# Kernel optimization log

Measured on AMD Instinct MI355X. Metric: run time of the kernel, lower is better.

Reference implementation:

```python
import jax, jax.numpy as jnp
import numpy as np

B, T, D = 64, 512, 2048
N = 16384            # buffer_size
ROUNDS = 10          # max_replay_rounds
DECAY = 0.9
THR = 0.5            # priority_threshold


def setup_inputs() -> dict:
    key = jax.random.key(0)
    ks = jax.random.split(key, 6)
    s = 0.02
    return {
        "query_states": jax.random.normal(ks[0], (B, T, D), jnp.float32),
        "attention_mask": jnp.ones((B, T), jnp.float32),
        "keys": jax.random.normal(ks[1], (N, D), jnp.float32),
        "values": jax.random.normal(ks[2], (N, D), jnp.float32),
        "priorities": jax.random.uniform(ks[3], (N,), jnp.float32),
        "ages": jnp.zeros((N,), jnp.float32),
        "valid_mask": jnp.ones((N,), jnp.bool_),
        "Wq": jax.random.normal(ks[4], (D, D), jnp.float32) * s,
        "bq": jnp.zeros((D,), jnp.float32),
        "Wc": jax.random.normal(ks[5], (D, D), jnp.float32) * s,
        "bc": jnp.zeros((D,), jnp.float32),
    }


def reference(query_states, attention_mask, keys, values, priorities, ages,
              valid_mask, Wq, bq, Wc, bc):
    # Masked mean-pool of context -> query  (B, D)
    m = attention_mask[..., None]
    query = (query_states * m).sum(axis=1) / (m.sum(axis=1) + 1e-8)
    query = query @ Wq.T + bq

    validf = valid_mask.astype(query.dtype)
    inv_sqrt_d = 1.0 / jnp.sqrt(jnp.asarray(D, query.dtype))
    base_scores = (query @ keys.T) * inv_sqrt_d  # (B, N), reused every round
    round_w = DECAY ** jnp.arange(ROUNDS, dtype=query.dtype)

    def step(carry, rw):
        w_ages, stopped, acc, wsum = carry
        eff = priorities * (DECAY ** w_ages)                       # (N,)
        active = jax.nn.sigmoid((eff - THR) * 10.0) * validf       # (N,)
        stopped = jnp.logical_or(stopped, active.sum() < 0.5)
        inc = jnp.where(stopped, 0.0, 1.0).astype(query.dtype)
        scores = base_scores * (active * eff)[None, :]             # (B, N)
        scores = jnp.where(valid_mask[None, :], scores, -jnp.inf)
        aw = jax.nn.softmax(scores, axis=-1)                       # (B, N)
        out = aw @ values                                          # (B, D)
        acc = acc + inc * rw * out
        wsum = wsum + inc * rw
        w_ages = w_ages + inc * jax.lax.stop_gradient(aw.mean(axis=0))
        return (w_ages, stopped, acc, wsum), None

    init = (ages, jnp.asarray(False), jnp.zeros((B, D), query.dtype),
            jnp.asarray(0.0, query.dtype))
    (w_ages, stopped, acc, wsum), _ = jax.lax.scan(step, init, round_w)

    # round_weights are normalized over the rounds actually executed
    consolidated = acc / jnp.maximum(wsum, 1e-8)
    consolidated = consolidated @ Wc.T + bc
    # if no round ran (or buffer empty), output is zeros (no projection)
    return jnp.where(wsum > 0, consolidated, jnp.zeros_like(consolidated))
```

## Files before the change

### kernel.cpp

```cpp
#include <hip/hip_runtime.h>
#include <math.h>

#define BB 64
#define TT 512
#define DD 2048
#define NBUF 16384
#define RND 10
#define DEC 0.9f
#define LN_DEC -0.10536051565782628f
#define THRV 0.5f
#define RBLK 64

constexpr size_t OFF_L    = 0;
constexpr size_t OFF_ASUM = OFF_L + (size_t)RND * BB;
constexpr size_t OFF_BAR  = OFF_ASUM + RND;
constexpr size_t ZERO_FLOATS = OFF_BAR + 4;
constexpr size_t OFF_ATOT = 656;
constexpr size_t OFF_BASE = OFF_ATOT + (size_t)BB * NBUF;
constexpr size_t OFF_ACC  = OFF_BASE + (size_t)BB * NBUF;
constexpr size_t OFF_POOL = OFF_ACC + (size_t)BB * DD;
constexpr size_t OFF_Q    = OFF_POOL + (size_t)BB * DD;
constexpr size_t OFF_MSUM = OFF_Q + (size_t)BB * DD;
constexpr size_t OFF_VLD  = OFF_MSUM + 64;
constexpr size_t OFF_PART = OFF_VLD + NBUF;
constexpr size_t WS_FLOATS = OFF_PART + (size_t)8 * BB * DD;

__device__ __forceinline__ float wave_sum(float v) {
#pragma unroll
  for (int o = 32; o; o >>= 1) v += __shfl_down(v, o);
  return v;
}

__device__ __forceinline__ float dev_wsum(const float* asum) {
  bool stopped = false; float w = 1.f, s = 0.f;
#pragma unroll
  for (int r = 0; r < RND; r++) {
    if (asum[r] < 0.5f) stopped = true;
    if (!stopped) s += w;
    w *= DEC;
  }
  return s;
}

__global__ __launch_bounds__(256) void k_valid(const void* __restrict__ valid, float* __restrict__ ws) {
  const unsigned char* vb = (const unsigned char*)valid;
  const unsigned int* vw = (const unsigned int*)valid;
  bool byte_layout = true;
#pragma unroll
  for (int i = 0; i < 16; i++) byte_layout = byte_layout && (vb[i] == (unsigned char)1);
  int n = blockIdx.x * 256 + threadIdx.x;
  float v = byte_layout ? (vb[n] ? 1.f : 0.f) : (vw[n] ? 1.f : 0.f);
  ws[OFF_VLD + n] = v;
}

__global__ __launch_bounds__(256) void k_msum(const float* __restrict__ mask, float* __restrict__ ws) {
  float* msum = ws + OFF_MSUM;
  int b = blockIdx.x, t = threadIdx.x;
  float s = mask[b * TT + t] + mask[b * TT + t + 256];
  s = wave_sum(s);
  __shared__ float red[4];
  if ((t & 63) == 0) red[t >> 6] = s;
  __syncthreads();
  if (t == 0) msum[b] = red[0] + red[1] + red[2] + red[3];
}

__global__ __launch_bounds__(256) void k_pool(const float* __restrict__ qs, const float* __restrict__ mask,
                                              float* __restrict__ ws) {
  float* part = ws + OFF_PART;
  int b = blockIdx.y;
  int d0 = blockIdx.x * 1024 + threadIdx.x * 4;
  int t0 = blockIdx.z * 64;
  __shared__ float ms[64];
  if (threadIdx.x < 64) ms[threadIdx.x] = mask[b * TT + t0 + threadIdx.x];
  __syncthreads();
  const float* p = qs + ((size_t)b * TT + t0) * DD + d0;
  float4 acc = make_float4(0.f, 0.f, 0.f, 0.f);
#pragma unroll 4
  for (int t = 0; t < 64; t++) {
    float m = ms[t];
    float4 v = *(const float4*)(p + (size_t)t * DD);
    acc.x = fmaf(v.x, m, acc.x); acc.y = fmaf(v.y, m, acc.y);
    acc.z = fmaf(v.z, m, acc.z); acc.w = fmaf(v.w, m, acc.w);
  }
  *(float4*)(part + ((size_t)blockIdx.z * BB + b) * DD + d0) = acc;
}

__global__ __launch_bounds__(256) void k_pooldiv(float* __restrict__ ws) {
  size_t i = (size_t)blockIdx.x * 256 + threadIdx.x;
  const float* part = ws + OFF_PART;
  const float* msum = ws + OFF_MSUM;
  float* pooled = ws + OFF_POOL;
  size_t BD = (size_t)BB * DD;
  float s = 0.f;
#pragma unroll
  for (int c = 0; c < 8; c++) s += part[c * BD + i];
  int b = (int)(i >> 11);
  pooled[i] = s / (msum[b] + 1e-8f);
}

__device__ __forceinline__ void stage_t(float* __restrict__ dst, const float* __restrict__ src, int ld) {
  int tr = threadIdx.x >> 2;
  int kb = (threadIdx.x & 3) << 4;
  const float* s = src + (size_t)tr * ld + kb;
#pragma unroll
  for (int q = 0; q < 4; q++) {
    float4 v = *(const float4*)(s + q * 4);
    int k = kb + q * 4;
    dst[(k + 0) * 68 + tr] = v.x;
    dst[(k + 1) * 68 + tr] = v.y;
    dst[(k + 2) * 68 + tr] = v.z;
    dst[(k + 3) * 68 + tr] = v.w;
  }
}

__device__ __forceinline__ void stage_t_bias(float* __restrict__ dst, const float* __restrict__ src, int ld,
                                             const float* __restrict__ bias) {
  int tr = threadIdx.x >> 2;
  int kb = (threadIdx.x & 3) << 4;
  const float* s = src + (size_t)tr * ld + kb;
#pragma unroll
  for (int q = 0; q < 4; q++) {
    float4 v = *(const float4*)(s + q * 4);
    float4 bv = *(const float4*)(bias + kb + q * 4);
    v.x += bv.x; v.y += bv.y; v.z += bv.z; v.w += bv.w;
    int k = kb + q * 4;
    dst[(k + 0) * 68 + tr] = v.x;
    dst[(k + 1) * 68 + tr] = v.y;
    dst[(k + 2) * 68 + tr] = v.z;
    dst[(k + 3) * 68 + tr] = v.w;
  }
}

__device__ __forceinline__ void stage_t_scale(float* __restrict__ dst, const float* __restrict__ src, int ld,
                                              float sc) {
  int tr = threadIdx.x >> 2;
  int kb = (threadIdx.x & 3) << 4;
  const float* s = src + (size_t)tr * ld + kb;
#pragma unroll
  for (int q = 0; q < 4; q++) {
    float4 v = *(const float4*)(s + q * 4);
    int k = kb + q * 4;
    dst[(k + 0) * 68 + tr] = v.x * sc;
    dst[(k + 1) * 68 + tr] = v.y * sc;
    dst[(k + 2) * 68 + tr] = v.z * sc;
    dst[(k + 3) * 68 + tr] = v.w * sc;
  }
}

__device__ __forceinline__ void stage_n(float* __restrict__ dst, const float* __restrict__ src, int ld) {
  int tr = threadIdx.x >> 2;
  int db = (threadIdx.x & 3) << 4;
  const float* s = src + (size_t)tr * ld + db;
  float* d = dst + tr * 68 + db;
#pragma unroll
  for (int q = 0; q < 4; q++) *(float4*)(d + q * 4) = *(const float4*)(s + q * 4);
}

__device__ __forceinline__ void gemm_core(const float* __restrict__ At, const float* __restrict__ Bt,
                                          float (&c)[4][4]) {
  const int tx = (threadIdx.x & 15) * 4;
  const int ty = (threadIdx.x >> 4) * 4;
#pragma unroll
  for (int k = 0; k < 64; k++) {
    float4 a = *(const float4*)(At + k * 68 + ty);
    float4 b = *(const float4*)(Bt + k * 68 + tx);
    c[0][0] = fmaf(a.x, b.x, c[0][0]); c[0][1] = fmaf(a.x, b.y, c[0][1]);
    c[0][2] = fmaf(a.x, b.z, c[0][2]); c[0][3] = fmaf(a.x, b.w, c[0][3]);
    c[1][0] = fmaf(a.y, b.x, c[1][0]); c[1][1] = fmaf(a.y, b.y, c[1][1]);
    c[1][2] = fmaf(a.y, b.z, c[1][2]); c[1][3] = fmaf(a.y, b.w, c[1][3]);
    c[2][0] = fmaf(a.z, b.x, c[2][0]); c[2][1] = fmaf(a.z, b.y, c[2][1]);
    c[2][2] = fmaf(a.z, b.z, c[2][2]); c[2][3] = fmaf(a.z, b.w, c[2][3]);
    c[3][0] = fmaf(a.w, b.x, c[3][0]); c[3][1] = fmaf(a.w, b.y, c[3][1]);
    c[3][2] = fmaf(a.w, b.z, c[3][2]); c[3][3] = fmaf(a.w, b.w, c[3][3]);
  }
}

__global__ __launch_bounds__(256) void k_wq(const float* __restrict__ Wq, float* __restrict__ ws) {
  __shared__ float At[64 * 68], Bt[64 * 68];
  const float* pooled = ws + OFF_POOL;
  float* part = ws + OFF_PART;
  int j0 = blockIdx.x * 64;
  int kc = blockIdx.y * 256;
  float c[4][4] = {};
  for (int kb = 0; kb < 256; kb += 64) {
    __syncthreads();
    stage_t(At, pooled + kc + kb, DD);
    stage_t(Bt, Wq + (size_t)j0 * DD + kc + kb, DD);
    __syncthreads();
    gemm_core(At, Bt, c);
  }
  int tx = (threadIdx.x & 15) * 4, ty = (threadIdx.x >> 4) * 4;
#pragma unroll
  for (int ii = 0; ii < 4; ii++) {
    float4 v = make_float4(c[ii][0], c[ii][1], c[ii][2], c[ii][3]);
    *(float4*)(part + ((size_t)blockIdx.y * BB + ty + ii) * DD + j0 + tx) = v;
  }
}

__global__ __launch_bounds__(256) void k_red8(float* __restrict__ dst, const float* __restrict__ ws) {
  size_t i = (size_t)blockIdx.x * 256 + threadIdx.x;
  const float* part = ws + OFF_PART;
  size_t BD = (size_t)BB * DD;
  float s = 0.f;
#pragma unroll
  for (int c = 0; c < 8; c++) s += part[c * BD + i];
  dst[i] = s;
}

__global__ __launch_bounds__(256) void k_base(const float* __restrict__ keys, const float* __restrict__ bq,
                                              float* __restrict__ ws) {
  __shared__ float At[64 * 68], Bt[64 * 68];
  const float* qacc = ws + OFF_Q;
  float* base = ws + OFF_BASE;
  int n0 = blockIdx.x * 64;
  float c[4][4] = {};
  for (int kb = 0; kb < DD; kb += 64) {
    __syncthreads();
    stage_t_bias(At, qacc + kb, DD, bq + kb);
    stage_t(Bt, keys + (size_t)n0 * DD + kb, DD);
    __syncthreads();
    gemm_core(At, Bt, c);
  }
  const float sc = 0.022097086912079608f;
  int tx = (threadIdx.x & 15) * 4, ty = (threadIdx.x >> 4) * 4;
#pragma unroll
  for (int ii = 0; ii < 4; ii++) {
    float4 v = make_float4(c[ii][0] * sc, c[ii][1] * sc, c[ii][2] * sc, c[ii][3] * sc);
    *(float4*)(base + (size_t)(ty + ii) * NBUF + n0 + tx) = v;
  }
}

__global__ __launch_bounds__(1024) void k_rounds(const float* __restrict__ prior,
                                                 const float* __restrict__ ages,
                                                 float* __restrict__ ws) {
  __shared__ float base_sh[64 * 256];
  __shared__ float wsh[256];
  __shared__ float red[4][256];
  __shared__ float red2[64][4];
  __shared__ float asq[4];
  __shared__ float rlsh[64];
  __shared__ float ash;
  float* lrow = ws + OFF_L;
  float* asum = ws + OFF_ASUM;
  unsigned int* bar = (unsigned int*)(ws + OFF_BAR);
  float* Atot = ws + OFF_ATOT;
  const float* base = ws + OFF_BASE;
  const float* vldbuf = ws + OFF_VLD;

  const int tid = threadIdx.x;
  const int nl = tid & 255, bq = tid >> 8;
  const int lane = tid & 63, sub = (tid >> 6) & 3;
  const int bx = blockIdx.x;
  const int n = bx * 256 + nl;

#pragma unroll
  for (int i = 0; i < 4; i++) {
    int f = (i * 1024 + tid) * 4;
    int b = f >> 8, c = f & 255;
    *(float4*)(base_sh + b * 256 + c) = *(const float4*)(base + (size_t)b * NBUF + bx * 256 + c);
  }
  if (tid < 256) wsh[tid] = ages[bx * 256 + tid];
  const float pv = prior[n];
  const float vld = vldbuf[n];
  float atot[16];
#pragma unroll
  for (int i = 0; i < 16; i++) atot[i] = 0.f;
  float w = 1.f;
  bool stopped = false;
  __syncthreads();

  for (int r = 0; r < RND; r++) {
    const float wa = wsh[nl];
    const float eff = pv * __expf(wa * LN_DEC);
    const float act = vld / (1.f + __expf(-10.f * (eff - THRV)));
    const float g = act * eff;
#pragma unroll
    for (int bi = 0; bi < 16; bi++) {
      const int b = bq * 16 + bi;
      float e = vld * __expf(base_sh[b * 256 + nl] * g);
      e = wave_sum(e);
      if (lane == 0) red2[b][sub] = e;
    }
    if (bq == 0) {
      float s = wave_sum(act);
      if (lane == 0) asq[sub] = s;
    }
    __syncthreads();
    if (tid < 64) {
      __hip_atomic_fetch_add(lrow + (size_t)r * BB + tid,
                             red2[tid][0] + red2[tid][1] + red2[tid][2] + red2[tid][3],
                             __ATOMIC_RELEASE, __HIP_MEMORY_SCOPE_AGENT);
    } else if (tid == 64) {
      __hip_atomic_fetch_add(asum + r, asq[0] + asq[1] + asq[2] + asq[3],
                             __ATOMIC_RELEASE, __HIP_MEMORY_SCOPE_AGENT);
    }
    __syncthreads();
    if (tid == 0) {
      __hip_atomic_fetch_add(bar, 1u, __ATOMIC_RELEASE, __HIP_MEMORY_SCOPE_AGENT);
      const unsigned int target = (unsigned int)RBLK * (unsigned int)(r + 1);
      while (__hip_atomic_load(bar, __ATOMIC_ACQUIRE, __HIP_MEMORY_SCOPE_AGENT) < target)
        __builtin_amdgcn_s_sleep(2);
    }
    __syncthreads();
    if (tid < 64)
      rlsh[tid] = 1.f / __hip_atomic_load(lrow + (size_t)r * BB + tid,
                                          __ATOMIC_RELAXED, __HIP_MEMORY_SCOPE_AGENT);
    else if (tid == 64)
      ash = __hip_atomic_load(asum + r, __ATOMIC_RELAXED, __HIP_MEMORY_SCOPE_AGENT);
    __syncthreads();
    stopped = stopped || (ash < 0.5f);
    const float coef = stopped ? 0.f : w;
    const float inc = stopped ? 0.f : 1.f;
    float csum = 0.f;
#pragma unroll
    for (int bi = 0; bi < 16; bi++) {
      const int b = bq * 16 + bi;
      const float e = vld * __expf(base_sh[b * 256 + nl] * g);
      const float aw = e * rlsh[b];
      atot[bi] = fmaf(coef, aw, atot[bi]);
      csum += aw;
    }
    red[bq][nl] = csum;
    __syncthreads();
    if (bq == 0)
      wsh[nl] = wa + inc * (red[0][nl] + red[1][nl] + red[2][nl] + red[3][nl]) * (1.f / 64.f);
    w *= DEC;
    __syncthreads();
  }
#pragma unroll
  for (int bi = 0; bi < 16; bi++) {
    const int b = bq * 16 + bi;
    Atot[(size_t)b * NBUF + n] = atot[bi];
  }
}

__global__ __launch_bounds__(256) void k_pv(const float* __restrict__ values, float* __restrict__ ws) {
  __shared__ float At[64 * 68], Bt[64 * 68];
  const float* Atot = ws + OFF_ATOT;
  float* part = ws + OFF_PART;
  int d0 = blockIdx.x * 64;
  int nc = blockIdx.y * 2048;
  float c[4][4] = {};
  for (int kb = 0; kb < 2048; kb += 64) {
    __syncthreads();
    stage_t(At, Atot + nc + kb, NBUF);
    stage_n(Bt, values + (size_t)(nc + kb) * DD + d0, DD);
    __syncthreads();
    gemm_core(At, Bt, c);
  }
  int tx = (threadIdx.x & 15) * 4, ty = (threadIdx.x >> 4) * 4;
#pragma unroll
  for (int ii = 0; ii < 4; ii++) {
    float4 v = make_float4(c[ii][0], c[ii][1], c[ii][2], c[ii][3]);
    *(float4*)(part + ((size_t)blockIdx.y * BB + ty + ii) * DD + d0 + tx) = v;
  }
}

__global__ __launch_bounds__(256) void k_wc(const float* __restrict__ Wc, float* __restrict__ ws) {
  __shared__ float At[64 * 68], Bt[64 * 68];
  const float* acc = ws + OFF_ACC;
  float rws = 1.f / fmaxf(dev_wsum(ws + OFF_ASUM), 1e-8f);
  float* part = ws + OFF_PART;
  int j0 = blockIdx.x * 64;
  int kc = blockIdx.y * 256;
  float c[4][4] = {};
  for (int kb = 0; kb < 256; kb += 64) {
    __syncthreads();
    stage_t_scale(At, acc + kc + kb, DD, rws);
    stage_t(Bt, Wc + (size_t)j0 * DD + kc + kb, DD);
    __syncthreads();
    gemm_core(At, Bt, c);
  }
  int tx = (threadIdx.x & 15) * 4, ty = (threadIdx.x >> 4) * 4;
#pragma unroll
  for (int ii = 0; ii < 4; ii++) {
    float4 v = make_float4(c[ii][0], c[ii][1], c[ii][2], c[ii][3]);
    *(float4*)(part + ((size_t)blockIdx.y * BB + ty + ii) * DD + j0 + tx) = v;
  }
}

__global__ __launch_bounds__(256) void k_red8_fin(float* __restrict__ out, const float* __restrict__ bc,
                                                  const float* __restrict__ ws) {
  size_t i = (size_t)blockIdx.x * 256 + threadIdx.x;
  const float* part = ws + OFF_PART;
  size_t BD = (size_t)BB * DD;
  float s = 0.f;
#pragma unroll
  for (int c = 0; c < 8; c++) s += part[c * BD + i];
  float wsv = dev_wsum(ws + OFF_ASUM);
  int j = (int)(i & (DD - 1));
  out[i] = (wsv > 0.f) ? (s + bc[j]) : 0.f;
}

extern "C" void kernel_launch(void* const* d_in, const int* in_sizes, int n_in,
                              void* d_out, int out_size, void* d_ws, size_t ws_size,
                              hipStream_t stream) {
  (void)in_sizes; (void)n_in; (void)out_size; (void)ws_size;
  const float* qs    = (const float*)d_in[0];
  const float* mask  = (const float*)d_in[1];
  const float* keys  = (const float*)d_in[2];
  const float* vals  = (const float*)d_in[3];
  const float* prior = (const float*)d_in[4];
  const float* ages  = (const float*)d_in[5];
  const void*  valid = (const void*)d_in[6];
  const float* Wq = (const float*)d_in[7];
  const float* bq = (const float*)d_in[8];
  const float* Wc = (const float*)d_in[9];
  const float* bc = (const float*)d_in[10];
  float* out = (float*)d_out;
  float* ws  = (float*)d_ws;

  hipMemsetAsync(ws, 0, ZERO_FLOATS * sizeof(float), stream);

  k_valid<<<NBUF / 256, 256, 0, stream>>>(valid, ws);
  k_msum<<<BB, 256, 0, stream>>>(mask, ws);
  k_pool<<<dim3(2, BB, 8), 256, 0, stream>>>(qs, mask, ws);
  k_pooldiv<<<(BB * DD) / 256, 256, 0, stream>>>(ws);
  k_wq<<<dim3(32, 8), 256, 0, stream>>>(Wq, ws);
  k_red8<<<(BB * DD) / 256, 256, 0, stream>>>(ws + OFF_Q, ws);
  k_base<<<NBUF / 64, 256, 0, stream>>>(keys, bq, ws);
  k_rounds<<<RBLK, 1024, 0, stream>>>(prior, ages, ws);
  k_pv<<<dim3(32, 8), 256, 0, stream>>>(vals, ws);
  k_red8<<<(BB * DD) / 256, 256, 0, stream>>>(ws + OFF_ACC, ws);
  k_wc<<<dim3(32, 8), 256, 0, stream>>>(Wc, ws);
  k_red8_fin<<<(BB * DD) / 256, 256, 0, stream>>>(out, bc, ws);
}
```

Baseline: 885.8 us.

## Split-K the base and PV GEMMs, vectorize reductions, merge init kernels

The keys GEMM is split four ways along K (4x more blocks), with a new reduction kernel that sums the partials and applies the scale. The PV GEMM's K split goes from 8 to 32 chunks, reduced by a new 32-way kernel. All partial-sum reductions now use float4 loads and stores, and the mask-sum and valid-conversion kernels are merged into one launch. The aim is better GPU occupancy on the two largest GEMMs and fewer launches, at the cost of extra workspace traffic for the partial buffers.

```diff
diff --git a/kernel.cpp b/kernel.cpp
--- a/kernel.cpp
+++ b/kernel.cpp
@@ -23,7 +23,8 @@
 constexpr size_t OFF_MSUM = OFF_Q + (size_t)BB * DD;
 constexpr size_t OFF_VLD  = OFF_MSUM + 64;
 constexpr size_t OFF_PART = OFF_VLD + NBUF;
-constexpr size_t WS_FLOATS = OFF_PART + (size_t)8 * BB * DD;
+constexpr size_t OFF_BPART= OFF_PART + (size_t)32 * BB * DD;
+constexpr size_t WS_FLOATS = OFF_BPART + (size_t)4 * BB * NBUF;
 
 __device__ __forceinline__ float wave_sum(float v) {
 #pragma unroll
@@ -42,26 +43,27 @@
   return s;
 }
 
-__global__ __launch_bounds__(256) void k_valid(const void* __restrict__ valid, float* __restrict__ ws) {
-  const unsigned char* vb = (const unsigned char*)valid;
-  const unsigned int* vw = (const unsigned int*)valid;
-  bool byte_layout = true;
-#pragma unroll
-  for (int i = 0; i < 16; i++) byte_layout = byte_layout && (vb[i] == (unsigned char)1);
-  int n = blockIdx.x * 256 + threadIdx.x;
-  float v = byte_layout ? (vb[n] ? 1.f : 0.f) : (vw[n] ? 1.f : 0.f);
-  ws[OFF_VLD + n] = v;
-}
-
-__global__ __launch_bounds__(256) void k_msum(const float* __restrict__ mask, float* __restrict__ ws) {
-  float* msum = ws + OFF_MSUM;
-  int b = blockIdx.x, t = threadIdx.x;
-  float s = mask[b * TT + t] + mask[b * TT + t + 256];
-  s = wave_sum(s);
-  __shared__ float red[4];
-  if ((t & 63) == 0) red[t >> 6] = s;
-  __syncthreads();
-  if (t == 0) msum[b] = red[0] + red[1] + red[2] + red[3];
+__global__ __launch_bounds__(256) void k_init(const float* __restrict__ mask, const void* __restrict__ valid,
+                                              float* __restrict__ ws) {
+  if (blockIdx.x < 64) {
+    float* msum = ws + OFF_MSUM;
+    int b = blockIdx.x, t = threadIdx.x;
+    float s = mask[b * TT + t] + mask[b * TT + t + 256];
+    s = wave_sum(s);
+    __shared__ float red[4];
+    if ((t & 63) == 0) red[t >> 6] = s;
+    __syncthreads();
+    if (t == 0) msum[b] = red[0] + red[1] + red[2] + red[3];
+  } else {
+    const unsigned char* vb = (const unsigned char*)valid;
+    const unsigned int* vw = (const unsigned int*)valid;
+    bool byte_layout = true;
+#pragma unroll
+    for (int i = 0; i < 16; i++) byte_layout = byte_layout && (vb[i] == (unsigned char)1);
+    int n = (blockIdx.x - 64) * 256 + threadIdx.x;
+    float v = byte_layout ? (vb[n] ? 1.f : 0.f) : (vw[n] ? 1.f : 0.f);
+    ws[OFF_VLD + n] = v;
+  }
 }
 
 __global__ __launch_bounds__(256) void k_pool(const float* __restrict__ qs, const float* __restrict__ mask,
@@ -86,16 +88,21 @@
 }
 
 __global__ __launch_bounds__(256) void k_pooldiv(float* __restrict__ ws) {
-  size_t i = (size_t)blockIdx.x * 256 + threadIdx.x;
-  const float* part = ws + OFF_PART;
+  size_t i4 = (size_t)blockIdx.x * 256 + threadIdx.x;
+  const float4* part = (const float4*)(ws + OFF_PART);
   const float* msum = ws + OFF_MSUM;
-  float* pooled = ws + OFF_POOL;
-  size_t BD = (size_t)BB * DD;
-  float s = 0.f;
-#pragma unroll
-  for (int c = 0; c < 8; c++) s += part[c * BD + i];
-  int b = (int)(i >> 11);
-  pooled[i] = s / (msum[b] + 1e-8f);
+  float4* pooled = (float4*)(ws + OFF_POOL);
+  size_t BD4 = (size_t)BB * DD / 4;
+  float4 s = make_float4(0.f, 0.f, 0.f, 0.f);
+#pragma unroll
+  for (int c = 0; c < 8; c++) {
+    float4 v = part[c * BD4 + i4];
+    s.x += v.x; s.y += v.y; s.z += v.z; s.w += v.w;
+  }
+  int b = (int)((i4 * 4) >> 11);
+  float r = 1.f / (msum[b] + 1e-8f);
+  s.x *= r; s.y *= r; s.z *= r; s.w *= r;
+  pooled[i4] = s;
 }
 
 __device__ __forceinline__ void stage_t(float* __restrict__ dst, const float* __restrict__ src, int ld) {
@@ -198,36 +205,55 @@
 }
 
 __global__ __launch_bounds__(256) void k_red8(float* __restrict__ dst, const float* __restrict__ ws) {
-  size_t i = (size_t)blockIdx.x * 256 + threadIdx.x;
-  const float* part = ws + OFF_PART;
-  size_t BD = (size_t)BB * DD;
-  float s = 0.f;
-#pragma unroll
-  for (int c = 0; c < 8; c++) s += part[c * BD + i];
-  dst[i] = s;
+  size_t i4 = (size_t)blockIdx.x * 256 + threadIdx.x;
+  const float4* part = (const float4*)(ws + OFF_PART);
+  size_t BD4 = (size_t)BB * DD / 4;
+  float4 s = make_float4(0.f, 0.f, 0.f, 0.f);
+#pragma unroll
+  for (int c = 0; c < 8; c++) {
+    float4 v = part[c * BD4 + i4];
+    s.x += v.x; s.y += v.y; s.z += v.z; s.w += v.w;
+  }
+  ((float4*)dst)[i4] = s;
 }
 
 __global__ __launch_bounds__(256) void k_base(const float* __restrict__ keys, const float* __restrict__ bq,
                                               float* __restrict__ ws) {
   __shared__ float At[64 * 68], Bt[64 * 68];
   const float* qacc = ws + OFF_Q;
-  float* base = ws + OFF_BASE;
+  float* bpart = ws + OFF_BPART;
   int n0 = blockIdx.x * 64;
+  int kc = blockIdx.y * 512;
   float c[4][4] = {};
-  for (int kb = 0; kb < DD; kb += 64) {
-    __syncthreads();
-    stage_t_bias(At, qacc + kb, DD, bq + kb);
-    stage_t(Bt, keys + (size_t)n0 * DD + kb, DD);
+  for (int kb = 0; kb < 512; kb += 64) {
+    __syncthreads();
+    stage_t_bias(At, qacc + kc + kb, DD, bq + kc + kb);
+    stage_t(Bt, keys + (size_t)n0 * DD + kc + kb, DD);
     __syncthreads();
     gemm_core(At, Bt, c);
   }
+  int tx = (threadIdx.x & 15) * 4, ty = (threadIdx.x >> 4) * 4;
+#pragma unroll
+  for (int ii = 0; ii < 4; ii++) {
+    float4 v = make_float4(c[ii][0], c[ii][1], c[ii][2], c[ii][3]);
+    *(float4*)(bpart + ((size_t)blockIdx.y * BB + ty + ii) * NBUF + n0 + tx) = v;
+  }
+}
+
+__global__ __launch_bounds__(256) void k_bred(float* __restrict__ ws) {
+  size_t i4 = (size_t)blockIdx.x * 256 + threadIdx.x;
+  const float4* bpart = (const float4*)(ws + OFF_BPART);
+  float4* base = (float4*)(ws + OFF_BASE);
+  size_t BN4 = (size_t)BB * NBUF / 4;
   const float sc = 0.022097086912079608f;
-  int tx = (threadIdx.x & 15) * 4, ty = (threadIdx.x >> 4) * 4;
-#pragma unroll
-  for (int ii = 0; ii < 4; ii++) {
-    float4 v = make_float4(c[ii][0] * sc, c[ii][1] * sc, c[ii][2] * sc, c[ii][3] * sc);
-    *(float4*)(base + (size_t)(ty + ii) * NBUF + n0 + tx) = v;
-  }
+  float4 s = make_float4(0.f, 0.f, 0.f, 0.f);
+#pragma unroll
+  for (int c = 0; c < 4; c++) {
+    float4 v = bpart[c * BN4 + i4];
+    s.x += v.x; s.y += v.y; s.z += v.z; s.w += v.w;
+  }
+  s.x *= sc; s.y *= sc; s.z *= sc; s.w *= sc;
+  base[i4] = s;
 }
 
 __global__ __launch_bounds__(1024) void k_rounds(const float* __restrict__ prior,
@@ -339,9 +365,9 @@
   const float* Atot = ws + OFF_ATOT;
   float* part = ws + OFF_PART;
   int d0 = blockIdx.x * 64;
-  int nc = blockIdx.y * 2048;
+  int nc = blockIdx.y * 512;
   float c[4][4] = {};
-  for (int kb = 0; kb < 2048; kb += 64) {
+  for (int kb = 0; kb < 512; kb += 64) {
     __syncthreads();
     stage_t(At, Atot + nc + kb, NBUF);
     stage_n(Bt, values + (size_t)(nc + kb) * DD + d0, DD);
@@ -354,6 +380,20 @@
     float4 v = make_float4(c[ii][0], c[ii][1], c[ii][2], c[ii][3]);
     *(float4*)(part + ((size_t)blockIdx.y * BB + ty + ii) * DD + d0 + tx) = v;
   }
+}
+
+__global__ __launch_bounds__(256) void k_red32(float* __restrict__ ws) {
+  size_t i4 = (size_t)blockIdx.x * 256 + threadIdx.x;
+  const float4* part = (const float4*)(ws + OFF_PART);
+  float4* acc = (float4*)(ws + OFF_ACC);
+  size_t BD4 = (size_t)BB * DD / 4;
+  float4 s = make_float4(0.f, 0.f, 0.f, 0.f);
+#pragma unroll
+  for (int c = 0; c < 32; c++) {
+    float4 v = part[c * BD4 + i4];
+    s.x += v.x; s.y += v.y; s.z += v.z; s.w += v.w;
+  }
+  acc[i4] = s;
 }
 
 __global__ __launch_bounds__(256) void k_wc(const float* __restrict__ Wc, float* __restrict__ ws) {
@@ -381,15 +421,25 @@
 
 __global__ __launch_bounds__(256) void k_red8_fin(float* __restrict__ out, const float* __restrict__ bc,
                                                   const float* __restrict__ ws) {
-  size_t i = (size_t)blockIdx.x * 256 + threadIdx.x;
-  const float* part = ws + OFF_PART;
-  size_t BD = (size_t)BB * DD;
-  float s = 0.f;
-#pragma unroll
-  for (int c = 0; c < 8; c++) s += part[c * BD + i];
+  size_t i4 = (size_t)blockIdx.x * 256 + threadIdx.x;
+  const float4* part = (const float4*)(ws + OFF_PART);
+  size_t BD4 = (size_t)BB * DD / 4;
+  float4 s = make_float4(0.f, 0.f, 0.f, 0.f);
+#pragma unroll
+  for (int c = 0; c < 8; c++) {
+    float4 v = part[c * BD4 + i4];
+    s.x += v.x; s.y += v.y; s.z += v.z; s.w += v.w;
+  }
   float wsv = dev_wsum(ws + OFF_ASUM);
-  int j = (int)(i & (DD - 1));
-  out[i] = (wsv > 0.f) ? (s + bc[j]) : 0.f;
+  int j0 = (int)((i4 * 4) & (DD - 1));
+  float4 bv = *(const float4*)(bc + j0);
+  float4 o;
+  if (wsv > 0.f) {
+    o.x = s.x + bv.x; o.y = s.y + bv.y; o.z = s.z + bv.z; o.w = s.w + bv.w;
+  } else {
+    o = make_float4(0.f, 0.f, 0.f, 0.f);
+  }
+  ((float4*)out)[i4] = o;
 }
 
 extern "C" void kernel_launch(void* const* d_in, const int* in_sizes, int n_in,
@@ -412,16 +462,16 @@
 
   hipMemsetAsync(ws, 0, ZERO_FLOATS * sizeof(float), stream);
 
-  k_valid<<<NBUF / 256, 256, 0, stream>>>(valid, ws);
-  k_msum<<<BB, 256, 0, stream>>>(mask, ws);
+  k_init<<<128, 256, 0, stream>>>(mask, valid, ws);
   k_pool<<<dim3(2, BB, 8), 256, 0, stream>>>(qs, mask, ws);
-  k_pooldiv<<<(BB * DD) / 256, 256, 0, stream>>>(ws);
+  k_pooldiv<<<(BB * DD / 4) / 256, 256, 0, stream>>>(ws);
   k_wq<<<dim3(32, 8), 256, 0, stream>>>(Wq, ws);
-  k_red8<<<(BB * DD) / 256, 256, 0, stream>>>(ws + OFF_Q, ws);
-  k_base<<<NBUF / 64, 256, 0, stream>>>(keys, bq, ws);
+  k_red8<<<(BB * DD / 4) / 256, 256, 0, stream>>>(ws + OFF_Q, ws);
+  k_base<<<dim3(NBUF / 64, 4), 256, 0, stream>>>(keys, bq, ws);
+  k_bred<<<(BB * NBUF / 4) / 256, 256, 0, stream>>>(ws);
   k_rounds<<<RBLK, 1024, 0, stream>>>(prior, ages, ws);
-  k_pv<<<dim3(32, 8), 256, 0, stream>>>(vals, ws);
-  k_red8<<<(BB * DD) / 256, 256, 0, stream>>>(ws + OFF_ACC, ws);
+  k_pv<<<dim3(DD / 64, 32), 256, 0, stream>>>(vals, ws);
+  k_red32<<<(BB * DD / 4) / 256, 256, 0, stream>>>(ws);
   k_wc<<<dim3(32, 8), 256, 0, stream>>>(Wc, ws);
-  k_red8_fin<<<(BB * DD) / 256, 256, 0, stream>>>(out, bc, ws);
-}
+  k_red8_fin<<<(BB * DD / 4) / 256, 256, 0, stream>>>(out, bc, ws);
+}
```

Measured after the change: 804.3 us. -9.2%, faster.
